# Performance work log

Hardware: AMD Instinct MI355X
Metric: run time of the kernel (lower is better)

Reference implementation:

```python
import jax, jax.numpy as jnp
import numpy as np


def setup_inputs() -> dict:
    key = jax.random.key(0)
    k1, k2, k3 = jax.random.split(key, 3)
    M, C, N, K, L = 4, 2, 512, 16000, 16
    mixture_w = jax.random.normal(k1, (M, N, K), dtype=jnp.float32)
    est_mask = jax.random.uniform(k2, (M, C, N, K), dtype=jnp.float32)
    W = jax.random.normal(k3, (L, N), dtype=jnp.float32) * (1.0 / np.sqrt(N))
    return {"mixture_w": mixture_w, "est_mask": est_mask, "W": W}


def reference(mixture_w, est_mask, W):
    # mixture_w: [M, N, K]; est_mask: [M, C, N, K]; W: [L, N] (torch Linear weight)
    L = W.shape[0]
    hop = L // 2
    source_w = mixture_w[:, None] * est_mask            # [M, C, N, K]
    frames = jnp.einsum('mcnk,ln->mckl', source_w, W)   # [M, C, K, L]
    M, C, K, Lf = frames.shape
    T = (K - 1) * hop + Lf
    # overlap-and-add: frame k writes to samples [k*hop, k*hop+L)
    idx = (jnp.arange(K)[:, None] * hop + jnp.arange(Lf)[None, :]).reshape(-1)
    est_source = jnp.zeros((M, C, T), frames.dtype).at[:, :, idx].add(
        frames.reshape(M, C, K * Lf))
    return est_source
```

## Files before the change

kernel.cpp:

```cpp
#include <hip/hip_runtime.h>


#define M_   4
#define C_   2
#define N_   512
#define K_   16000
#define L_   16
#define HOP  8
#define T_   ((K_ - 1) * HOP + L_)
#define BK   64
#define NSEG 4
#define NPW  (N_ / NSEG)
#define NCH  (NPW / 4)
#define NB   (K_ / BK)
#define GRID (M_ * NB)
#define RSTRIDE 20
#define WS_TAIL_OFF (M_ * C_ * NB * 8)

__global__ __launch_bounds__(256, 4)
void decoder_kernel(const float* __restrict__ mix,
                    const float* __restrict__ mask,
                    const float* __restrict__ Wg,
                    float* __restrict__ out,
                    float* __restrict__ ws) {
    __shared__ float lds[3 * 64 * RSTRIDE];

    const int tid  = threadIdx.x;
    const int lane = tid & 63;
    const int w    = tid >> 6;
    const int m    = blockIdx.x / NB;
    const int bb   = blockIdx.x % NB;
    const int k0   = bb * BK;

    float acc0[16], acc1[16];
    #pragma unroll
    for (int i = 0; i < 16; ++i) { acc0[i] = 0.f; acc1[i] = 0.f; }

    const int n0w  = w * NPW;
    const int n0wU = __builtin_amdgcn_readfirstlane(n0w);
    const int kk   = k0 + lane;

    const float* pm = mix  + (size_t)m * N_ * K_ + (size_t)n0w * K_ + kk;
    const float* p0 = mask + ((size_t)(m * C_) * N_ + n0w) * K_ + kk;
    const float* p1 = p0 + (size_t)N_ * K_;

    #pragma unroll 2
    for (int ch = 0; ch < NCH; ++ch) {
        float mv[4], a0[4], a1[4];
        #pragma unroll
        for (int j = 0; j < 4; ++j) {
            mv[j] = pm[(size_t)j * K_];
            a0[j] = p0[(size_t)j * K_];
            a1[j] = p1[(size_t)j * K_];
        }
        float s0[4], s1[4];
        #pragma unroll
        for (int j = 0; j < 4; ++j) { s0[j] = mv[j] * a0[j]; s1[j] = mv[j] * a1[j]; }

        const int nbase = n0wU + ch * 4;
        #pragma unroll
        for (int l = 0; l < L_; ++l) {
            const float4 w4 = *(const float4*)&Wg[l * N_ + nbase];
            acc0[l] = fmaf(s0[0], w4.x, acc0[l]);
            acc0[l] = fmaf(s0[1], w4.y, acc0[l]);
            acc0[l] = fmaf(s0[2], w4.z, acc0[l]);
            acc0[l] = fmaf(s0[3], w4.w, acc0[l]);
            acc1[l] = fmaf(s1[0], w4.x, acc1[l]);
            acc1[l] = fmaf(s1[1], w4.y, acc1[l]);
            acc1[l] = fmaf(s1[2], w4.z, acc1[l]);
            acc1[l] = fmaf(s1[3], w4.w, acc1[l]);
        }
        pm += (size_t)4 * K_;
        p0 += (size_t)4 * K_;
        p1 += (size_t)4 * K_;
    }

    auto reduce_c = [&](float (&acc)[16]) {
        __syncthreads();
        if (w > 0) {
            float* rb = &lds[(w - 1) * (64 * RSTRIDE) + lane * RSTRIDE];
            #pragma unroll
            for (int i = 0; i < 4; ++i)
                *(float4*)&rb[i * 4] = make_float4(acc[i*4], acc[i*4+1],
                                                   acc[i*4+2], acc[i*4+3]);
        }
        __syncthreads();
        if (w == 0) {
            #pragma unroll
            for (int r = 0; r < 3; ++r) {
                const float* rb = &lds[r * (64 * RSTRIDE) + lane * RSTRIDE];
                #pragma unroll
                for (int i = 0; i < 4; ++i) {
                    const float4 v = *(const float4*)&rb[i * 4];
                    acc[i*4]   += v.x;  acc[i*4+1] += v.y;
                    acc[i*4+2] += v.z;  acc[i*4+3] += v.w;
                }
            }
        }
    };
    reduce_c(acc0);
    reduce_c(acc1);

    if (w == 0) {
#define EPILOGUE(ACC, CIDX)                                                   \
        {                                                                     \
            float* ob = out + (size_t)(m * C_ + (CIDX)) * T_                  \
                            + (size_t)kk * HOP;                               \
            float cmb[8];                                                     \
            _Pragma("unroll")                                                 \
            for (int j = 0; j < 8; ++j) {                                     \
                const float pv = __shfl_up(ACC[8 + j], 1);                    \
                cmb[j] = ACC[j] + pv;                                         \
            }                                                                 \
            if (lane == 0) {                                                  \
                float* hb = ws + (size_t)((m * C_ + (CIDX)) * NB + bb) * 8;   \
                *(float4*)&hb[0] = make_float4(ACC[0], ACC[1], ACC[2], ACC[3]);\
                *(float4*)&hb[4] = make_float4(ACC[4], ACC[5], ACC[6], ACC[7]);\
            } else {                                                          \
                *(float4*)&ob[0] = make_float4(cmb[0], cmb[1], cmb[2], cmb[3]);\
                *(float4*)&ob[4] = make_float4(cmb[4], cmb[5], cmb[6], cmb[7]);\
            }                                                                 \
            if (lane == 63) {                                                 \
                float* tb = ws + WS_TAIL_OFF                                  \
                             + (size_t)((m * C_ + (CIDX)) * NB + bb) * 8;     \
                *(float4*)&tb[0] = make_float4(ACC[8],  ACC[9],               \
                                               ACC[10], ACC[11]);             \
                *(float4*)&tb[4] = make_float4(ACC[12], ACC[13],              \
                                               ACC[14], ACC[15]);             \
            }                                                                 \
        }
        EPILOGUE(acc0, 0)
        EPILOGUE(acc1, 1)
#undef EPILOGUE
    }
}

__global__ __launch_bounds__(256)
void boundary_kernel(const float* __restrict__ ws, float* __restrict__ out) {
    const int id = blockIdx.x * 256 + threadIdx.x;
    const int total = M_ * C_ * NB * 8;
    if (id >= total) return;
    const int j  = id & 7;
    const int bb = (id >> 3) % NB;
    const int mc = (id >> 3) / NB;
    float v = ws[(size_t)(mc * NB + bb) * 8 + j];
    if (bb > 0) v += ws[WS_TAIL_OFF + (size_t)(mc * NB + bb - 1) * 8 + j];
    out[(size_t)mc * T_ + (size_t)bb * (BK * HOP) + j] = v;
    if (bb == NB - 1) {
        out[(size_t)mc * T_ + (size_t)K_ * HOP + j] =
            ws[WS_TAIL_OFF + (size_t)(mc * NB + bb) * 8 + j];
    }
}

extern "C" void kernel_launch(void* const* d_in, const int* in_sizes, int n_in,
                              void* d_out, int out_size, void* d_ws, size_t ws_size,
                              hipStream_t stream) {
    const float* mix  = (const float*)d_in[0];
    const float* mask = (const float*)d_in[1];
    const float* Wg   = (const float*)d_in[2];
    float* out = (float*)d_out;
    float* ws  = (float*)d_ws;

    decoder_kernel<<<dim3(GRID), dim3(256), 0, stream>>>(mix, mask, Wg, out, ws);
    boundary_kernel<<<dim3((M_ * C_ * NB * 8 + 255) / 256), dim3(256), 0, stream>>>(ws, out);
}
```

Baseline: 88.05 us.

## Process two adjacent frames per lane with float2 loads and 8 N-segments

Each lane now handles two consecutive frames (even/odd) using float2 loads, doubling the block's K tile to 128. The N reduction is split across 8 wavefronts in 512-thread blocks, with a wider LDS reduction buffer. Within a lane, the even/odd frame overlap is combined directly in registers. The aim is to reuse each W load across twice as many FMAs and widen global loads. In exchange it roughly doubles accumulator registers, halves the grid size, and lengthens the serial LDS reduction in wave 0.

```diff
diff --git a/kernel.cpp b/kernel.cpp
--- a/kernel.cpp
+++ b/kernel.cpp
@@ -8,22 +8,22 @@
 #define L_   16
 #define HOP  8
 #define T_   ((K_ - 1) * HOP + L_)
-#define BK   64
-#define NSEG 4
+#define BK   128
+#define NSEG 8
 #define NPW  (N_ / NSEG)
 #define NCH  (NPW / 4)
 #define NB   (K_ / BK)
 #define GRID (M_ * NB)
-#define RSTRIDE 20
+#define RSTRIDE 36
 #define WS_TAIL_OFF (M_ * C_ * NB * 8)
 
-__global__ __launch_bounds__(256, 4)
+__global__ __launch_bounds__(512, 4)
 void decoder_kernel(const float* __restrict__ mix,
                     const float* __restrict__ mask,
                     const float* __restrict__ Wg,
                     float* __restrict__ out,
                     float* __restrict__ ws) {
-    __shared__ float lds[3 * 64 * RSTRIDE];
+    __shared__ float lds[7 * 64 * RSTRIDE];
 
     const int tid  = threadIdx.x;
     const int lane = tid & 63;
@@ -32,105 +32,127 @@
     const int bb   = blockIdx.x % NB;
     const int k0   = bb * BK;
 
-    float acc0[16], acc1[16];
+    float accE0[16], accO0[16], accE1[16], accO1[16];
     #pragma unroll
-    for (int i = 0; i < 16; ++i) { acc0[i] = 0.f; acc1[i] = 0.f; }
+    for (int i = 0; i < 16; ++i) {
+        accE0[i] = 0.f; accO0[i] = 0.f; accE1[i] = 0.f; accO1[i] = 0.f;
+    }
 
     const int n0w  = w * NPW;
     const int n0wU = __builtin_amdgcn_readfirstlane(n0w);
-    const int kk   = k0 + lane;
+    const int kk   = k0 + 2 * lane;
 
     const float* pm = mix  + (size_t)m * N_ * K_ + (size_t)n0w * K_ + kk;
     const float* p0 = mask + ((size_t)(m * C_) * N_ + n0w) * K_ + kk;
     const float* p1 = p0 + (size_t)N_ * K_;
 
-    #pragma unroll 2
     for (int ch = 0; ch < NCH; ++ch) {
-        float mv[4], a0[4], a1[4];
+        float2 mv[4], a0[4], a1[4];
         #pragma unroll
         for (int j = 0; j < 4; ++j) {
-            mv[j] = pm[(size_t)j * K_];
-            a0[j] = p0[(size_t)j * K_];
-            a1[j] = p1[(size_t)j * K_];
+            mv[j] = *(const float2*)&pm[(size_t)j * K_];
+            a0[j] = *(const float2*)&p0[(size_t)j * K_];
+            a1[j] = *(const float2*)&p1[(size_t)j * K_];
         }
-        float s0[4], s1[4];
+        float sE0[4], sO0[4], sE1[4], sO1[4];
         #pragma unroll
-        for (int j = 0; j < 4; ++j) { s0[j] = mv[j] * a0[j]; s1[j] = mv[j] * a1[j]; }
-
+        for (int j = 0; j < 4; ++j) {
+            sE0[j] = mv[j].x * a0[j].x;  sO0[j] = mv[j].y * a0[j].y;
+            sE1[j] = mv[j].x * a1[j].x;  sO1[j] = mv[j].y * a1[j].y;
+        }
         const int nbase = n0wU + ch * 4;
         #pragma unroll
         for (int l = 0; l < L_; ++l) {
             const float4 w4 = *(const float4*)&Wg[l * N_ + nbase];
-            acc0[l] = fmaf(s0[0], w4.x, acc0[l]);
-            acc0[l] = fmaf(s0[1], w4.y, acc0[l]);
-            acc0[l] = fmaf(s0[2], w4.z, acc0[l]);
-            acc0[l] = fmaf(s0[3], w4.w, acc0[l]);
-            acc1[l] = fmaf(s1[0], w4.x, acc1[l]);
-            acc1[l] = fmaf(s1[1], w4.y, acc1[l]);
-            acc1[l] = fmaf(s1[2], w4.z, acc1[l]);
-            acc1[l] = fmaf(s1[3], w4.w, acc1[l]);
+            const float wv[4] = { w4.x, w4.y, w4.z, w4.w };
+            #pragma unroll
+            for (int j = 0; j < 4; ++j) {
+                accE0[l] = fmaf(sE0[j], wv[j], accE0[l]);
+                accO0[l] = fmaf(sO0[j], wv[j], accO0[l]);
+                accE1[l] = fmaf(sE1[j], wv[j], accE1[l]);
+                accO1[l] = fmaf(sO1[j], wv[j], accO1[l]);
+            }
         }
         pm += (size_t)4 * K_;
         p0 += (size_t)4 * K_;
         p1 += (size_t)4 * K_;
     }
 
-    auto reduce_c = [&](float (&acc)[16]) {
-        __syncthreads();
-        if (w > 0) {
-            float* rb = &lds[(w - 1) * (64 * RSTRIDE) + lane * RSTRIDE];
-            #pragma unroll
-            for (int i = 0; i < 4; ++i)
-                *(float4*)&rb[i * 4] = make_float4(acc[i*4], acc[i*4+1],
-                                                   acc[i*4+2], acc[i*4+3]);
-        }
-        __syncthreads();
-        if (w == 0) {
-            #pragma unroll
-            for (int r = 0; r < 3; ++r) {
-                const float* rb = &lds[r * (64 * RSTRIDE) + lane * RSTRIDE];
-                #pragma unroll
-                for (int i = 0; i < 4; ++i) {
-                    const float4 v = *(const float4*)&rb[i * 4];
-                    acc[i*4]   += v.x;  acc[i*4+1] += v.y;
-                    acc[i*4+2] += v.z;  acc[i*4+3] += v.w;
-                }
-            }
-        }
-    };
-    reduce_c(acc0);
-    reduce_c(acc1);
+#define REDUCE_C(AE, AO)                                                      \
+    {                                                                         \
+        __syncthreads();                                                      \
+        if (w > 0) {                                                          \
+            float* rb = &lds[(w - 1) * (64 * RSTRIDE) + lane * RSTRIDE];      \
+            _Pragma("unroll")                                                 \
+            for (int i = 0; i < 4; ++i)                                       \
+                *(float4*)&rb[i * 4] = make_float4(AE[i*4], AE[i*4+1],        \
+                                                   AE[i*4+2], AE[i*4+3]);     \
+            _Pragma("unroll")                                                 \
+            for (int i = 0; i < 4; ++i)                                       \
+                *(float4*)&rb[16 + i * 4] = make_float4(AO[i*4], AO[i*4+1],   \
+                                                        AO[i*4+2], AO[i*4+3]);\
+        }                                                                     \
+        __syncthreads();                                                      \
+        if (w == 0) {                                                         \
+            _Pragma("unroll")                                                 \
+            for (int r = 0; r < 7; ++r) {                                     \
+                const float* rb = &lds[r * (64 * RSTRIDE) + lane * RSTRIDE];  \
+                _Pragma("unroll")                                             \
+                for (int i = 0; i < 4; ++i) {                                 \
+                    const float4 v = *(const float4*)&rb[i * 4];              \
+                    AE[i*4]   += v.x;  AE[i*4+1] += v.y;                      \
+                    AE[i*4+2] += v.z;  AE[i*4+3] += v.w;                      \
+                }                                                             \
+                _Pragma("unroll")                                             \
+                for (int i = 0; i < 4; ++i) {                                 \
+                    const float4 v = *(const float4*)&rb[16 + i * 4];         \
+                    AO[i*4]   += v.x;  AO[i*4+1] += v.y;                      \
+                    AO[i*4+2] += v.z;  AO[i*4+3] += v.w;                      \
+                }                                                             \
+            }                                                                 \
+        }                                                                     \
+    }
+    REDUCE_C(accE0, accO0)
+    REDUCE_C(accE1, accO1)
+#undef REDUCE_C
 
     if (w == 0) {
-#define EPILOGUE(ACC, CIDX)                                                   \
+#define EPILOGUE(AE, AO, CIDX)                                                \
         {                                                                     \
             float* ob = out + (size_t)(m * C_ + (CIDX)) * T_                  \
                             + (size_t)kk * HOP;                               \
-            float cmb[8];                                                     \
+            float cmbE[8], cmbO[8];                                           \
             _Pragma("unroll")                                                 \
             for (int j = 0; j < 8; ++j) {                                     \
-                const float pv = __shfl_up(ACC[8 + j], 1);                    \
-                cmb[j] = ACC[j] + pv;                                         \
+                const float pv = __shfl_up(AO[8 + j], 1);                     \
+                cmbE[j] = AE[j] + pv;                  \
+                cmbO[j] = AO[j] + AE[8 + j];                     \
             }                                                                 \
             if (lane == 0) {                                                  \
                 float* hb = ws + (size_t)((m * C_ + (CIDX)) * NB + bb) * 8;   \
-                *(float4*)&hb[0] = make_float4(ACC[0], ACC[1], ACC[2], ACC[3]);\
-                *(float4*)&hb[4] = make_float4(ACC[4], ACC[5], ACC[6], ACC[7]);\
+                *(float4*)&hb[0] = make_float4(AE[0], AE[1], AE[2], AE[3]);   \
+                *(float4*)&hb[4] = make_float4(AE[4], AE[5], AE[6], AE[7]);   \
             } else {                                                          \
-                *(float4*)&ob[0] = make_float4(cmb[0], cmb[1], cmb[2], cmb[3]);\
-                *(float4*)&ob[4] = make_float4(cmb[4], cmb[5], cmb[6], cmb[7]);\
+                *(float4*)&ob[0] = make_float4(cmbE[0], cmbE[1],              \
+                                               cmbE[2], cmbE[3]);             \
+                *(float4*)&ob[4] = make_float4(cmbE[4], cmbE[5],              \
+                                               cmbE[6], cmbE[7]);             \
             }                                                                 \
+            *(float4*)&ob[8]  = make_float4(cmbO[0], cmbO[1],                 \
+                                            cmbO[2], cmbO[3]);                \
+            *(float4*)&ob[12] = make_float4(cmbO[4], cmbO[5],                 \
+                                            cmbO[6], cmbO[7]);                \
             if (lane == 63) {                                                 \
                 float* tb = ws + WS_TAIL_OFF                                  \
                              + (size_t)((m * C_ + (CIDX)) * NB + bb) * 8;     \
-                *(float4*)&tb[0] = make_float4(ACC[8],  ACC[9],               \
-                                               ACC[10], ACC[11]);             \
-                *(float4*)&tb[4] = make_float4(ACC[12], ACC[13],              \
-                                               ACC[14], ACC[15]);             \
+                *(float4*)&tb[0] = make_float4(AO[8],  AO[9],                 \
+                                               AO[10], AO[11]);               \
+                *(float4*)&tb[4] = make_float4(AO[12], AO[13],                \
+                                               AO[14], AO[15]);               \
             }                                                                 \
         }
-        EPILOGUE(acc0, 0)
-        EPILOGUE(acc1, 1)
+        EPILOGUE(accE0, accO0, 0)
+        EPILOGUE(accE1, accO1, 1)
 #undef EPILOGUE
     }
 }
@@ -161,6 +183,6 @@
     float* out = (float*)d_out;
     float* ws  = (float*)d_ws;
 
-    decoder_kernel<<<dim3(GRID), dim3(256), 0, stream>>>(mix, mask, Wg, out, ws);
+    decoder_kernel<<<dim3(GRID), dim3(512), 0, stream>>>(mix, mask, Wg, out, ws);
     boundary_kernel<<<dim3((M_ * C_ * NB * 8 + 255) / 256), dim3(256), 0, stream>>>(ws, out);
 }
```

Result: slower. 99.82 us (+13.4%).
